# Optimization experiments

Hardware: AMD Instinct MI355X
Metric: run time of the kernel (lower is better)

Reference implementation:

```python
import jax, jax.numpy as jnp
import numpy as np

GROUPS = 16
GROUP_SIZE = 16
K = 3
KK = K * K
BN_EPS = 1e-5


def setup_inputs() -> dict:
    key = jax.random.key(0)
    ks = jax.random.split(key, 6)
    B, C, H, W = 16, 256, 56, 56
    mid = C // 4  # rd_ratio = 4
    x = jax.random.normal(ks[0], (B, C, H, W), dtype=jnp.float32)
    w1 = jax.random.normal(ks[1], (mid, C), dtype=jnp.float32) * (1.0 / np.sqrt(C))
    bn_gamma = jnp.ones((mid,), dtype=jnp.float32)
    bn_beta = jnp.zeros((mid,), dtype=jnp.float32)
    bn_mean = jax.random.normal(ks[2], (mid,), dtype=jnp.float32) * 0.1
    bn_var = jax.random.uniform(ks[3], (mid,), dtype=jnp.float32, minval=0.5, maxval=1.5)
    w2 = jax.random.normal(ks[4], (KK * GROUPS, mid), dtype=jnp.float32) * (1.0 / np.sqrt(mid))
    b2 = jax.random.normal(ks[5], (KK * GROUPS,), dtype=jnp.float32) * 0.01
    return {"x": x, "w1": w1, "bn_gamma": bn_gamma, "bn_beta": bn_beta,
            "bn_mean": bn_mean, "bn_var": bn_var, "w2": w2, "b2": b2}


def reference(x, w1, bn_gamma, bn_beta, bn_mean, bn_var, w2, b2):
    B, C, H, W = x.shape
    # conv1: 1x1 conv + BatchNorm (eval) + ReLU
    t = jnp.einsum('bchw,oc->bohw', x, w1)
    scale = bn_gamma / jnp.sqrt(bn_var + BN_EPS)
    t = t * scale[None, :, None, None] + (bn_beta - bn_mean * scale)[None, :, None, None]
    t = jax.nn.relu(t)
    # conv2: 1x1 conv producing per-pixel kernels (B, KK*groups, H, W)
    weight = jnp.einsum('bchw,oc->bohw', t, w2) + b2[None, :, None, None]
    weight = weight.reshape(B, GROUPS, 1, KK, H, W)
    # unfold: extract 3x3 patches (pad=1, stride=1), kernel positions row-major
    xp = jnp.pad(x, ((0, 0), (0, 0), (1, 1), (1, 1)))
    patches = jnp.stack(
        [xp[:, :, i:i + H, j:j + W] for i in range(K) for j in range(K)],
        axis=2)  # (B, C, KK, H, W), matches torch unfold's (c*KK + kk) layout
    patches = patches.reshape(B, GROUPS, GROUP_SIZE, KK, H, W)
    out = (weight * patches).sum(axis=3).reshape(B, C, H, W)
    return out
```

## Files before the change

kernel.cpp:

```cpp
#include <hip/hip_runtime.h>


#define Cn    256
#define MID   64
#define Hn    56
#define Wn    56
#define HW    3136
#define Bn    16
#define NPIX  (Bn * HW)
#define CHW   (Cn * HW)
#define NKK   9
#define NG    16
#define GSZ   16
#define PXT   64
#define BN_EPS 1e-5f

__global__ __launch_bounds__(256) void prep_kernel(
    const float* __restrict__ w1,
    const float* __restrict__ gamma,
    const float* __restrict__ beta,
    const float* __restrict__ mean,
    const float* __restrict__ var,
    float* __restrict__ w1f,
    float* __restrict__ bias1) {
  int idx = blockIdx.x * 256 + threadIdx.x;
  if (idx < MID * Cn) {
    int c = idx >> 6;
    int o = idx & 63;
    float scale = gamma[o] / sqrtf(var[o] + BN_EPS);
    w1f[idx] = w1[o * Cn + c] * scale;
  } else if (idx < MID * Cn + MID) {
    int o = idx - MID * Cn;
    float scale = gamma[o] / sqrtf(var[o] + BN_EPS);
    bias1[o] = beta[o] - mean[o] * scale;
  }
}

__global__ __launch_bounds__(256) void conv1_kernel(
    const float* __restrict__ x,
    const float* __restrict__ w1f,
    const float* __restrict__ bias1,
    float* __restrict__ t) {
  __shared__ float lx[2][16][PXT];

  int tid = threadIdx.x;
  int px  = tid & 63;
  int ocv = tid >> 6;
  int oc  = __builtin_amdgcn_readfirstlane(ocv);

  int px0 = blockIdx.x * PXT;
  int b   = px0 / HW;
  int hw0 = px0 - b * HW;
  const float* xb = x + (size_t)b * CHW + hw0;

  float r[4];
#pragma unroll
  for (int j = 0; j < 4; ++j) {
    int c = j * 4 + ocv;
    r[j] = xb[(size_t)c * HW + px];
  }
#pragma unroll
  for (int j = 0; j < 4; ++j) lx[0][j * 4 + ocv][px] = r[j];
  __syncthreads();

  float acc[16];
#pragma unroll
  for (int j = 0; j < 16; ++j) acc[j] = 0.0f;

  for (int k = 0; k < 16; ++k) {
    int cur = k & 1;
    if (k < 15) {
#pragma unroll
      for (int j = 0; j < 4; ++j) {
        int c = (k + 1) * 16 + j * 4 + ocv;
        r[j] = xb[(size_t)c * HW + px];
      }
    }
#pragma unroll
    for (int c = 0; c < 16; ++c) {
      float xv = lx[cur][c][px];
      const float* wr = w1f + ((k * 16 + c) << 6) + (oc << 4);
#pragma unroll
      for (int q = 0; q < 4; ++q) {
        float4 w4 = *(const float4*)(wr + q * 4);
        acc[q * 4 + 0] = fmaf(xv, w4.x, acc[q * 4 + 0]);
        acc[q * 4 + 1] = fmaf(xv, w4.y, acc[q * 4 + 1]);
        acc[q * 4 + 2] = fmaf(xv, w4.z, acc[q * 4 + 2]);
        acc[q * 4 + 3] = fmaf(xv, w4.w, acc[q * 4 + 3]);
      }
    }
    if (k < 15) {
#pragma unroll
      for (int j = 0; j < 4; ++j) lx[1 - cur][j * 4 + ocv][px] = r[j];
    }
    __syncthreads();
  }

#pragma unroll
  for (int j = 0; j < 16; ++j) {
    int o = oc * 16 + j;
    float v = acc[j] + bias1[o];
    t[(size_t)o * NPIX + px0 + px] = fmaxf(v, 0.0f);
  }
}

__global__ __launch_bounds__(256) void conv2_inv_kernel(
    const float* __restrict__ x,
    const float* __restrict__ t,
    const float* __restrict__ w2,
    const float* __restrict__ b2,
    float* __restrict__ out) {
  __shared__ float lt[MID][PXT];
  __shared__ float lw[NG * NKK][PXT];

  int tid = threadIdx.x;
  int px  = tid & 63;
  int wvv = tid >> 6;
  int wvu = __builtin_amdgcn_readfirstlane(wvv);

  int px0 = blockIdx.x * PXT;
  int b   = px0 / HW;
  int hw0 = px0 - b * HW;

#pragma unroll
  for (int j = 0; j < 16; ++j) {
    int o = j * 4 + wvv;
    lt[o][px] = t[(size_t)o * NPIX + px0 + px];
  }
  __syncthreads();

  for (int gi = 0; gi < 4; ++gi) {
    int g = wvu + gi * 4;
    float a[NKK];
#pragma unroll
    for (int kk = 0; kk < NKK; ++kk) a[kk] = b2[g * NKK + kk];
#pragma unroll 4
    for (int o = 0; o < MID; ++o) {
      float tv = lt[o][px];
      const float* w2o = w2 + o;
#pragma unroll
      for (int kk = 0; kk < NKK; ++kk)
        a[kk] = fmaf(tv, w2o[(g * NKK + kk) * MID], a[kk]);
    }
#pragma unroll
    for (int kk = 0; kk < NKK; ++kk) lw[g * NKK + kk][px] = a[kk];
  }
  __syncthreads();

  int hw = hw0 + px;
  int h  = hw / Wn;
  int w  = hw - h * Wn;

  int off[NKK];
  unsigned vmask = 0;
#pragma unroll
  for (int kk = 0; kk < NKK; ++kk) {
    int di = kk / 3 - 1;
    int dj = kk % 3 - 1;
    int h2 = h + di;
    int w2v = w + dj;
    bool valid = ((unsigned)h2 < (unsigned)Hn) && ((unsigned)w2v < (unsigned)Wn);
    off[kk] = valid ? (h2 * Wn + w2v) : hw;
    vmask |= (valid ? 1u : 0u) << kk;
  }

  const float* xb = x + (size_t)b * CHW;
  float* ob = out + (size_t)b * CHW + hw;

  for (int gi = 0; gi < 4; ++gi) {
    int g = wvu + gi * 4;
    float wk[NKK];
#pragma unroll
    for (int kk = 0; kk < NKK; ++kk)
      wk[kk] = ((vmask >> kk) & 1u) ? lw[g * NKK + kk][px] : 0.0f;

#pragma unroll 4
    for (int cc = 0; cc < GSZ; ++cc) {
      int c = g * GSZ + cc;
      const float* xc = xb + (size_t)c * HW;
      float a = 0.0f;
#pragma unroll
      for (int kk = 0; kk < NKK; ++kk)
        a = fmaf(wk[kk], xc[off[kk]], a);
      ob[(size_t)c * HW] = a;
    }
  }
}

extern "C" void kernel_launch(void* const* d_in, const int* in_sizes, int n_in,
                              void* d_out, int out_size, void* d_ws, size_t ws_size,
                              hipStream_t stream) {
  const float* x     = (const float*)d_in[0];
  const float* w1    = (const float*)d_in[1];
  const float* gamma = (const float*)d_in[2];
  const float* beta  = (const float*)d_in[3];
  const float* mean  = (const float*)d_in[4];
  const float* var   = (const float*)d_in[5];
  const float* w2    = (const float*)d_in[6];
  const float* b2    = (const float*)d_in[7];
  float* out = (float*)d_out;

  char* ws = (char*)d_ws;
  float* t     = (float*)ws;
  float* w1f   = (float*)(ws + (size_t)MID * NPIX * 4);
  float* bias1 = (float*)(ws + (size_t)MID * NPIX * 4 + (size_t)MID * Cn * 4);

  prep_kernel<<<(MID * Cn + MID + 255) / 256, 256, 0, stream>>>(
      w1, gamma, beta, mean, var, w1f, bias1);
  conv1_kernel<<<NPIX / PXT, 256, 0, stream>>>(x, w1f, bias1, t);
  conv2_inv_kernel<<<NPIX / PXT, 256, 0, stream>>>(x, t, w2, b2, out);
}
```

Baseline: 194.2 us.

## Double threads per block and keep conv2 kernel weights in registers

Both conv kernels now launch 512 threads (8 waves) per 64-pixel tile. Each wave handles half as many output channels in conv1 and two groups in conv2, with launch bounds hinting higher occupancy. In conv2, the transposed t tile is stored in padded LDS and read with float4. The per-pixel 3x3 weights are computed with per-wave dot products and kept in registers rather than round-tripping through shared memory, and the unfold loads are batched four channels at a time for more memory-level parallelism. The aim is more latency hiding and less LDS traffic, at the cost of higher register pressure and duplicated weight loads per wave.

```diff
diff --git a/kernel.cpp b/kernel.cpp
--- a/kernel.cpp
+++ b/kernel.cpp
@@ -13,6 +13,7 @@
 #define NG    16
 #define GSZ   16
 #define PXT   64
+#define LTP   68
 #define BN_EPS 1e-5f
 
 __global__ __launch_bounds__(256) void prep_kernel(
@@ -36,7 +37,7 @@
   }
 }
 
-__global__ __launch_bounds__(256) void conv1_kernel(
+__global__ __launch_bounds__(512, 8) void conv1_kernel(
     const float* __restrict__ x,
     const float* __restrict__ w1f,
     const float* __restrict__ bias1,
@@ -50,38 +51,32 @@
 
   int px0 = blockIdx.x * PXT;
   int b   = px0 / HW;
-  int hw0 = px0 - b * HW;
-  const float* xb = x + (size_t)b * CHW + hw0;
-
-  float r[4];
-#pragma unroll
-  for (int j = 0; j < 4; ++j) {
-    int c = j * 4 + ocv;
-    r[j] = xb[(size_t)c * HW + px];
-  }
-#pragma unroll
-  for (int j = 0; j < 4; ++j) lx[0][j * 4 + ocv][px] = r[j];
+  const float* xb = x + (size_t)b * CHW + (px0 - b * HW) + px;
+
+  float r[2];
+#pragma unroll
+  for (int j = 0; j < 2; ++j) r[j] = xb[(size_t)(ocv * 2 + j) * HW];
+#pragma unroll
+  for (int j = 0; j < 2; ++j) lx[0][ocv * 2 + j][px] = r[j];
   __syncthreads();
 
-  float acc[16];
-#pragma unroll
-  for (int j = 0; j < 16; ++j) acc[j] = 0.0f;
+  float acc[8];
+#pragma unroll
+  for (int j = 0; j < 8; ++j) acc[j] = 0.0f;
 
   for (int k = 0; k < 16; ++k) {
     int cur = k & 1;
     if (k < 15) {
 #pragma unroll
-      for (int j = 0; j < 4; ++j) {
-        int c = (k + 1) * 16 + j * 4 + ocv;
-        r[j] = xb[(size_t)c * HW + px];
-      }
+      for (int j = 0; j < 2; ++j)
+        r[j] = xb[(size_t)((k + 1) * 16 + ocv * 2 + j) * HW];
     }
 #pragma unroll
     for (int c = 0; c < 16; ++c) {
       float xv = lx[cur][c][px];
-      const float* wr = w1f + ((k * 16 + c) << 6) + (oc << 4);
-#pragma unroll
-      for (int q = 0; q < 4; ++q) {
+      const float* wr = w1f + ((k * 16 + c) << 6) + (oc << 3);
+#pragma unroll
+      for (int q = 0; q < 2; ++q) {
         float4 w4 = *(const float4*)(wr + q * 4);
         acc[q * 4 + 0] = fmaf(xv, w4.x, acc[q * 4 + 0]);
         acc[q * 4 + 1] = fmaf(xv, w4.y, acc[q * 4 + 1]);
@@ -91,27 +86,25 @@
     }
     if (k < 15) {
 #pragma unroll
-      for (int j = 0; j < 4; ++j) lx[1 - cur][j * 4 + ocv][px] = r[j];
+      for (int j = 0; j < 2; ++j) lx[1 - cur][ocv * 2 + j][px] = r[j];
     }
     __syncthreads();
   }
 
 #pragma unroll
-  for (int j = 0; j < 16; ++j) {
-    int o = oc * 16 + j;
-    float v = acc[j] + bias1[o];
-    t[(size_t)o * NPIX + px0 + px] = fmaxf(v, 0.0f);
-  }
-}
-
-__global__ __launch_bounds__(256) void conv2_inv_kernel(
+  for (int j = 0; j < 8; ++j) {
+    int o = oc * 8 + j;
+    t[(size_t)o * NPIX + px0 + px] = fmaxf(acc[j] + bias1[o], 0.0f);
+  }
+}
+
+__global__ __launch_bounds__(512, 5) void conv2_inv_kernel(
     const float* __restrict__ x,
     const float* __restrict__ t,
     const float* __restrict__ w2,
     const float* __restrict__ b2,
     float* __restrict__ out) {
-  __shared__ float lt[MID][PXT];
-  __shared__ float lw[NG * NKK][PXT];
+  __shared__ float lt[PXT][LTP];
 
   int tid = threadIdx.x;
   int px  = tid & 63;
@@ -123,29 +116,45 @@
   int hw0 = px0 - b * HW;
 
 #pragma unroll
-  for (int j = 0; j < 16; ++j) {
-    int o = j * 4 + wvv;
-    lt[o][px] = t[(size_t)o * NPIX + px0 + px];
+  for (int j = 0; j < 8; ++j) {
+    int o = wvv * 8 + j;
+    lt[px][o] = t[(size_t)o * NPIX + px0 + px];
   }
   __syncthreads();
 
-  for (int gi = 0; gi < 4; ++gi) {
-    int g = wvu + gi * 4;
-    float a[NKK];
-#pragma unroll
-    for (int kk = 0; kk < NKK; ++kk) a[kk] = b2[g * NKK + kk];
-#pragma unroll 4
-    for (int o = 0; o < MID; ++o) {
-      float tv = lt[o][px];
-      const float* w2o = w2 + o;
-#pragma unroll
-      for (int kk = 0; kk < NKK; ++kk)
-        a[kk] = fmaf(tv, w2o[(g * NKK + kk) * MID], a[kk]);
-    }
-#pragma unroll
-    for (int kk = 0; kk < NKK; ++kk) lw[g * NKK + kk][px] = a[kk];
-  }
-  __syncthreads();
+  float a[2][9];
+#pragma unroll
+  for (int gi = 0; gi < 2; ++gi)
+#pragma unroll
+    for (int kk = 0; kk < NKK; ++kk)
+      a[gi][kk] = b2[(wvu * 2 + gi) * NKK + kk];
+
+#pragma unroll
+  for (int half = 0; half < 2; ++half) {
+    float tr[32];
+#pragma unroll
+    for (int q = 0; q < 8; ++q)
+      *(float4*)&tr[q * 4] = *(const float4*)&lt[px][half * 32 + q * 4];
+
+#pragma unroll
+    for (int gi = 0; gi < 2; ++gi) {
+      int g = wvu * 2 + gi;
+#pragma unroll
+      for (int kk = 0; kk < NKK; ++kk) {
+        const float4* wr = (const float4*)(w2 + (g * NKK + kk) * MID + half * 32);
+        float s = a[gi][kk];
+#pragma unroll
+        for (int q = 0; q < 8; ++q) {
+          float4 w4 = wr[q];
+          s = fmaf(tr[q * 4 + 0], w4.x, s);
+          s = fmaf(tr[q * 4 + 1], w4.y, s);
+          s = fmaf(tr[q * 4 + 2], w4.z, s);
+          s = fmaf(tr[q * 4 + 3], w4.w, s);
+        }
+        a[gi][kk] = s;
+      }
+    }
+  }
 
   int hw = hw0 + px;
   int h  = hw / Wn;
@@ -167,22 +176,33 @@
   const float* xb = x + (size_t)b * CHW;
   float* ob = out + (size_t)b * CHW + hw;
 
-  for (int gi = 0; gi < 4; ++gi) {
-    int g = wvu + gi * 4;
+#pragma unroll
+  for (int gi = 0; gi < 2; ++gi) {
+    int g = wvu * 2 + gi;
     float wk[NKK];
 #pragma unroll
     for (int kk = 0; kk < NKK; ++kk)
-      wk[kk] = ((vmask >> kk) & 1u) ? lw[g * NKK + kk][px] : 0.0f;
-
-#pragma unroll 4
-    for (int cc = 0; cc < GSZ; ++cc) {
-      int c = g * GSZ + cc;
-      const float* xc = xb + (size_t)c * HW;
-      float a = 0.0f;
-#pragma unroll
-      for (int kk = 0; kk < NKK; ++kk)
-        a = fmaf(wk[kk], xc[off[kk]], a);
-      ob[(size_t)c * HW] = a;
+      wk[kk] = ((vmask >> kk) & 1u) ? a[gi][kk] : 0.0f;
+
+    const float* xg = xb + (size_t)(g * GSZ) * HW;
+#pragma unroll
+    for (int c4 = 0; c4 < 4; ++c4) {
+      float xv[4][NKK];
+#pragma unroll
+      for (int cc = 0; cc < 4; ++cc) {
+        const float* xc = xg + (size_t)(c4 * 4 + cc) * HW;
+#pragma unroll
+        for (int kk = 0; kk < NKK; ++kk)
+          xv[cc][kk] = xc[off[kk]];
+      }
+#pragma unroll
+      for (int cc = 0; cc < 4; ++cc) {
+        float s = 0.0f;
+#pragma unroll
+        for (int kk = 0; kk < NKK; ++kk)
+          s = fmaf(wk[kk], xv[cc][kk], s);
+        ob[(size_t)(g * GSZ + c4 * 4 + cc) * HW] = s;
+      }
     }
   }
 }
@@ -207,6 +227,6 @@
 
   prep_kernel<<<(MID * Cn + MID + 255) / 256, 256, 0, stream>>>(
       w1, gamma, beta, mean, var, w1f, bias1);
-  conv1_kernel<<<NPIX / PXT, 256, 0, stream>>>(x, w1f, bias1, t);
-  conv2_inv_kernel<<<NPIX / PXT, 256, 0, stream>>>(x, t, w2, b2, out);
-}
+  conv1_kernel<<<NPIX / PXT, 512, 0, stream>>>(x, w1f, bias1, t);
+  conv2_inv_kernel<<<NPIX / PXT, 512, 0, stream>>>(x, t, w2, b2, out);
+}
```

Result: slower. 217.2 us (+11.8%).
